# Kernel tuning notes

Measured on AMD Instinct MI355X. Metric: run time of the kernel, lower is better.

Reference implementation:

```python
import jax, jax.numpy as jnp
import numpy as np

WS = 7            # window size
HEADS = 4
DIM = 128         # hidden_dim
HEAD_DIM = 128    # wrapper passes head_dim=hidden_dim (faithful to source)
INNER = HEADS * HEAD_DIM   # 512
MLP = 4 * DIM
PATCH = 4
DISP = WS // 2
NEG = -1e9


def _ln(x, g, b, eps=1e-5):
    m = jnp.mean(x, -1, keepdims=True)
    v = jnp.mean((x - m) ** 2, -1, keepdims=True)
    return (x - m) * jax.lax.rsqrt(v + eps) * g + b


_coords = np.stack(np.meshgrid(np.arange(WS), np.arange(WS), indexing='ij'), -1).reshape(-1, 2)
REL_IDX = jnp.asarray(_coords[None] - _coords[:, None] + WS - 1)  # (ws^2, ws^2, 2)


def _build_masks():
    n = WS * WS
    ul = np.zeros((n, n), np.float32)
    ul[-DISP * WS:, : -DISP * WS] = NEG
    ul[: -DISP * WS, -DISP * WS:] = NEG
    lr = np.zeros((WS, WS, WS, WS), np.float32)
    lr[:, -DISP:, :, : -DISP] = NEG
    lr[:, : -DISP, :, -DISP:] = NEG
    return jnp.asarray(ul), jnp.asarray(lr.reshape(n, n))

UL_MASK, LR_MASK = _build_masks()


def _win_attn(x, w_qkv, pos, w_o, b_o, shifted):
    b, H, W, _ = x.shape
    if shifted:
        x = jnp.roll(x, (-DISP, -DISP), axis=(1, 2))
    nh, nw = H // WS, W // WS
    qkv = x @ w_qkv  # (b, H, W, 3*INNER)

    def to_win(t):  # -> (b, heads, n_windows, ws*ws, head_dim)
        t = t.reshape(b, nh, WS, nw, WS, HEADS, HEAD_DIM)
        return t.transpose(0, 5, 1, 3, 2, 4, 6).reshape(b, HEADS, nh * nw, WS * WS, HEAD_DIM)

    q, k, v = map(to_win, jnp.split(qkv, 3, axis=-1))
    dots = jnp.einsum('bhwid,bhwjd->bhwij', q, k) * (HEAD_DIM ** -0.5)
    dots = dots + pos[REL_IDX[..., 0], REL_IDX[..., 1]]  # shared across heads (berniwal)
    if shifted:
        dots = dots.at[:, :, -nw:].add(UL_MASK)
        dots = dots.at[:, :, nw - 1::nw].add(LR_MASK)
    attn = jax.nn.softmax(dots, axis=-1)
    out = jnp.einsum('bhwij,bhwjd->bhwid', attn, v)
    out = out.reshape(b, HEADS, nh, nw, WS, WS, HEAD_DIM).transpose(0, 2, 4, 3, 5, 1, 6)
    out = out.reshape(b, H, W, INNER) @ w_o + b_o
    if shifted:
        out = jnp.roll(out, (DISP, DISP), axis=(1, 2))
    return out


def _block(x, ga1, be1, w_qkv, pos, w_o, b_o, ga2, be2, w1, b1, w2, b2, shifted):
    x = x + _win_attn(_ln(x, ga1, be1), w_qkv, pos, w_o, b_o, shifted)
    h = jax.nn.gelu(_ln(x, ga2, be2) @ w1 + b1, approximate=False) @ w2 + b2
    return x + h


def _patch_embed(x, w, b):  # Unfold(patch) + Linear, channel-major feature order
    B, C, H, W = x.shape
    nh, nw = H // PATCH, W // PATCH
    x = x.reshape(B, C, nh, PATCH, nw, PATCH).transpose(0, 2, 4, 1, 3, 5)
    return x.reshape(B, nh, nw, C * PATCH * PATCH) @ w + b


def setup_inputs() -> dict:
    key = jax.random.key(0)
    ks = iter(jax.random.split(key, 48))

    def nrm(shape, s=0.02):
        return jax.random.normal(next(ks), shape, dtype=jnp.float32) * s

    inp = {'x': jax.random.normal(next(ks), (32, 3, 224, 224), dtype=jnp.float32)}
    inp['w_pe'] = nrm((3 * PATCH * PATCH, DIM))
    inp['b_pe'] = jnp.zeros((DIM,), jnp.float32)
    for s in ('a', 'b'):
        inp['ga1_' + s] = jnp.ones((DIM,), jnp.float32)
        inp['be1_' + s] = jnp.zeros((DIM,), jnp.float32)
        inp['w_qkv_' + s] = nrm((DIM, 3 * INNER))
        inp['pos_' + s] = nrm((2 * WS - 1, 2 * WS - 1), 1.0)
        inp['w_o_' + s] = nrm((INNER, DIM))
        inp['b_o_' + s] = jnp.zeros((DIM,), jnp.float32)
        inp['ga2_' + s] = jnp.ones((DIM,), jnp.float32)
        inp['be2_' + s] = jnp.zeros((DIM,), jnp.float32)
        inp['w_m1_' + s] = nrm((DIM, MLP))
        inp['b_m1_' + s] = jnp.zeros((MLP,), jnp.float32)
        inp['w_m2_' + s] = nrm((MLP, DIM))
        inp['b_m2_' + s] = jnp.zeros((DIM,), jnp.float32)
    return inp


def reference(x, w_pe, b_pe,
              ga1_a, be1_a, w_qkv_a, pos_a, w_o_a, b_o_a, ga2_a, be2_a, w_m1_a, b_m1_a, w_m2_a, b_m2_a,
              ga1_b, be1_b, w_qkv_b, pos_b, w_o_b, b_o_b, ga2_b, be2_b, w_m1_b, b_m1_b, w_m2_b, b_m2_b):
    h = _patch_embed(x, w_pe, b_pe)  # (B, 56, 56, DIM)
    h = _block(h, ga1_a, be1_a, w_qkv_a, pos_a, w_o_a, b_o_a, ga2_a, be2_a, w_m1_a, b_m1_a, w_m2_a, b_m2_a, False)
    h = _block(h, ga1_b, be1_b, w_qkv_b, pos_b, w_o_b, b_o_b, ga2_b, be2_b, w_m1_b, b_m1_b, w_m2_b, b_m2_b, True)
    return h
```

## Files before the change

### kernel.cpp

```cpp
#include <hip/hip_runtime.h>

typedef __attribute__((ext_vector_type(8))) short bf16x8;
typedef __attribute__((ext_vector_type(4))) short bf16x4;
typedef __attribute__((ext_vector_type(4))) float f32x4;

#define MFMA16(a, b, c) __builtin_amdgcn_mfma_f32_16x16x32_bf16(a, b, c, 0, 0, 0)

static __device__ __forceinline__ short f2bf(float f) {
    union { float f; unsigned u; } x; x.f = f;
    unsigned r = x.u + 0x7FFFu + ((x.u >> 16) & 1u);
    return (short)(r >> 16);
}

static __device__ __forceinline__ void gload16(const void* g, void* l) {
    __builtin_amdgcn_global_load_lds((const __attribute__((address_space(1))) void*)g,
                                     (__attribute__((address_space(3))) void*)l, 16, 0, 0);
}

__global__ void convT_kernel(const float* __restrict__ in, short* __restrict__ out, int K, int N) {
    int idx = blockIdx.x * 256 + threadIdx.x;
    if (idx < K * N) {
        int k = idx % K, n = idx / K;
        out[idx] = f2bf(in[(size_t)k * N + n]);
    }
}

__global__ void tabgen_kernel(const float* __restrict__ pos_a, const float* __restrict__ pos_b,
                              float* __restrict__ tab) {
    int v = blockIdx.x;
    const float* pos = (v == 0) ? pos_a : pos_b;
    for (int e = threadIdx.x; e < 4096; e += 256) {
        int row = e >> 6, key = e & 63;
        float val;
        if (key >= 49) val = -1e9f;
        else if (row >= 49) val = 0.f;
        else {
            int qi = row / 7, qj = row - qi * 7, ki = key / 7, kj = key - ki * 7;
            val = pos[(ki - qi + 6) * 13 + (kj - qj + 6)];
            if (v >= 1) {
                bool wh7 = (v - 1) & 2, ww7 = (v - 1) & 1;
                if (wh7 && ((qi >= 4) != (ki >= 4))) val += -1e9f;
                if (ww7 && ((qj >= 4) != (kj >= 4))) val += -1e9f;
            }
        }
        tab[v * 4096 + e] = val;
    }
}

__global__ __launch_bounds__(256) void patchln_kernel(const float* __restrict__ x,
                                                      const float* __restrict__ w,
                                                      const float* __restrict__ bias,
                                                      const float* __restrict__ g,
                                                      const float* __restrict__ bta,
                                                      float* __restrict__ out,
                                                      short* __restrict__ xn) {
    __shared__ float s_in[2][48];
    __shared__ float red[2][2][2];
    const int tid = threadIdx.x;
    const int half = tid >> 7, c = tid & 127;
    const int winh = (tid >> 6) & 1, lane = tid & 63;
    const int t = blockIdx.x * 2 + half;
    const int b = t / 3136, rem = t - b * 3136;
    const int hp = rem / 56, wp = rem - hp * 56;
    if (c < 48) {
        int cin = c >> 4, py = (c >> 2) & 3, px = c & 3;
        s_in[half][c] = x[((size_t)(b * 3 + cin) * 224 + hp * 4 + py) * 224 + wp * 4 + px];
    }
    __syncthreads();
    float acc = bias[c];
#pragma unroll
    for (int k = 0; k < 48; ++k) acc += s_in[half][k] * w[k * 128 + c];
    out[(size_t)t * 128 + c] = acc;
    float s1 = acc, s2 = acc * acc;
#pragma unroll
    for (int o = 32; o > 0; o >>= 1) { s1 += __shfl_xor(s1, o); s2 += __shfl_xor(s2, o); }
    if (lane == 0) { red[half][winh][0] = s1; red[half][winh][1] = s2; }
    __syncthreads();
    s1 = red[half][0][0] + red[half][1][0];
    s2 = red[half][0][1] + red[half][1][1];
    float mean = s1 * (1.f / 128.f);
    float var = s2 * (1.f / 128.f) - mean * mean;
    float rstd = rsqrtf(var + 1e-5f);
    xn[(size_t)t * 128 + c] = f2bf((acc - mean) * rstd * g[c] + bta[c]);
}

template <int SHIFTED>
__global__ __launch_bounds__(256, 3) void attn_kernel(const short* __restrict__ xn,
                                                      const short* __restrict__ wqkvT,
                                                      const float* __restrict__ tab,
                                                      const short* __restrict__ zpad,
                                                      short* __restrict__ aout) {
    __shared__ short smem[24576];
    short* s_x = smem;
    short* s_q = smem + 8192;
    short* s_k = smem + 16384;
    short* s_vT = smem + 8192;
    short* s_p = smem + 16384;

    const int tid = threadIdx.x;
    const int wid = tid >> 6, lane = tid & 63;
    const int l15 = lane & 15, l4 = lane >> 4, klo = l4 * 8;
    const int bid = blockIdx.x;
    const int win = bid & 63, head = (bid >> 6) & 3, b = bid >> 8;
    const int wh = win >> 3, ww = win & 7;

#pragma unroll
    for (int it = 0; it < 4; ++it) {
        int slot = it * 256 + tid;
        int row = slot >> 4, scol = slot & 15;
        int colb = (scol * 16) ^ ((row & 7) << 4);
        const char* g;
        if (row < 49) {
            int wi = row / 7, wj = row - wi * 7;
            int hh = wh * 7 + wi, wp = ww * 7 + wj;
            if (SHIFTED) { hh += 3; if (hh >= 56) hh -= 56; wp += 3; if (wp >= 56) wp -= 56; }
            int t = (b * 56 + hh) * 56 + wp;
            g = (const char*)(xn + (size_t)t * 128) + colb;
        } else {
            g = (const char*)zpad + colb;
        }
        gload16(g, (char*)smem + (it * 256 + wid * 64) * 16);
    }
    __syncthreads();

    const f32x4 zero4 = {0.f, 0.f, 0.f, 0.f};

    {
        const short* Wq = wqkvT + (size_t)(head * 128) * 128;
        const short* Wk = wqkvT + (size_t)(512 + head * 128) * 128;
        f32x4 aq[2][4], ak[2][4];
#pragma unroll
        for (int mw = 0; mw < 2; ++mw)
#pragma unroll
            for (int j = 0; j < 4; ++j) { aq[mw][j] = zero4; ak[mw][j] = zero4; }
#pragma unroll
        for (int k0 = 0; k0 < 4; ++k0) {
            bf16x8 bx[4], awq[2], awk[2];
#pragma unroll
            for (int j = 0; j < 4; ++j) {
                int row = j * 16 + l15;
                bx[j] = *(const bf16x8*)((const char*)s_x + row * 256 + ((k0 * 64 + l4 * 16) ^ ((row & 7) << 4)));
            }
#pragma unroll
            for (int mw = 0; mw < 2; ++mw) {
                awq[mw] = *(const bf16x8*)(Wq + (size_t)(wid * 32 + mw * 16 + l15) * 128 + k0 * 32 + klo);
                awk[mw] = *(const bf16x8*)(Wk + (size_t)(wid * 32 + mw * 16 + l15) * 128 + k0 * 32 + klo);
            }
            __builtin_amdgcn_s_setprio(1);
#pragma unroll
            for (int mw = 0; mw < 2; ++mw)
#pragma unroll
                for (int j = 0; j < 4; ++j) {
                    aq[mw][j] = MFMA16(awq[mw], bx[j], aq[mw][j]);
                    ak[mw][j] = MFMA16(awk[mw], bx[j], ak[mw][j]);
                }
            __builtin_amdgcn_s_setprio(0);
        }
#pragma unroll
        for (int mw = 0; mw < 2; ++mw)
#pragma unroll
            for (int j = 0; j < 4; ++j) {
                bf16x4 pq, pk;
#pragma unroll
                for (int r = 0; r < 4; ++r) { pq[r] = f2bf(aq[mw][j][r]); pk[r] = f2bf(ak[mw][j][r]); }
                int row = j * 16 + l15;
                int colb = (wid * 64 + mw * 32 + l4 * 8) ^ ((row & 7) << 4);
                *(bf16x4*)((char*)s_q + row * 256 + colb) = pq;
                *(bf16x4*)((char*)s_k + row * 256 + colb) = pk;
            }
    }
    __syncthreads();

    const int qrow = wid * 16 + l15;
    f32x4 dt[4];
#pragma unroll
    for (int m = 0; m < 4; ++m) dt[m] = zero4;
#pragma unroll
    for (int k0 = 0; k0 < 4; ++k0) {
        bf16x8 bq = *(const bf16x8*)((const char*)s_q + qrow * 256 + ((k0 * 64 + l4 * 16) ^ ((qrow & 7) << 4)));
        __builtin_amdgcn_s_setprio(1);
#pragma unroll
        for (int m = 0; m < 4; ++m) {
            int krow = m * 16 + l15;
            bf16x8 akf = *(const bf16x8*)((const char*)s_k + krow * 256 + ((k0 * 64 + l4 * 16) ^ ((krow & 7) << 4)));
            dt[m] = MFMA16(akf, bq, dt[m]);
        }
        __builtin_amdgcn_s_setprio(0);
    }
    __syncthreads();

    const int variant = SHIFTED ? (1 + ((wh == 7) ? 2 : 0) + ((ww == 7) ? 1 : 0)) : 0;
    const float* tv = tab + variant * 4096 + qrow * 64;
    const float SC = 0.08838834764831845f;
    float p[4][4];
    float mx = -3.0e38f;
#pragma unroll
    for (int m = 0; m < 4; ++m) {
        f32x4 tb = *(const f32x4*)(tv + m * 16 + l4 * 4);
#pragma unroll
        for (int r = 0; r < 4; ++r) {
            float d = dt[m][r] * SC + tb[r];
            p[m][r] = d;
            mx = fmaxf(mx, d);
        }
    }
    mx = fmaxf(mx, __shfl_xor(mx, 16));
    mx = fmaxf(mx, __shfl_xor(mx, 32));
    float sum = 0.f;
#pragma unroll
    for (int m = 0; m < 4; ++m)
#pragma unroll
        for (int r = 0; r < 4; ++r) { p[m][r] = __expf(p[m][r] - mx); sum += p[m][r]; }
    sum += __shfl_xor(sum, 16);
    sum += __shfl_xor(sum, 32);
    float inv = 1.f / sum;
#pragma unroll
    for (int m = 0; m < 4; ++m) {
        bf16x4 pv;
#pragma unroll
        for (int r = 0; r < 4; ++r) pv[r] = f2bf(p[m][r] * inv);
        *(bf16x4*)((char*)s_p + qrow * 128 + ((m * 32 + l4 * 8) ^ ((qrow & 7) << 4))) = pv;
    }

    {
        const short* Wv = wqkvT + (size_t)(1024 + head * 128) * 128;
        f32x4 acc[4][2];
#pragma unroll
        for (int m = 0; m < 4; ++m)
#pragma unroll
            for (int n = 0; n < 2; ++n) acc[m][n] = zero4;
#pragma unroll
        for (int k0 = 0; k0 < 4; ++k0) {
            bf16x8 ax[4], bw[2];
#pragma unroll
            for (int m = 0; m < 4; ++m) {
                int row = m * 16 + l15;
                ax[m] = *(const bf16x8*)((const char*)s_x + row * 256 + ((k0 * 64 + l4 * 16) ^ ((row & 7) << 4)));
            }
#pragma unroll
            for (int n = 0; n < 2; ++n)
                bw[n] = *(const bf16x8*)(Wv + (size_t)(wid * 32 + n * 16 + l15) * 128 + k0 * 32 + klo);
            __builtin_amdgcn_s_setprio(1);
#pragma unroll
            for (int m = 0; m < 4; ++m)
#pragma unroll
                for (int n = 0; n < 2; ++n) acc[m][n] = MFMA16(ax[m], bw[n], acc[m][n]);
            __builtin_amdgcn_s_setprio(0);
        }
#pragma unroll
        for (int m = 0; m < 4; ++m)
#pragma unroll
            for (int n = 0; n < 2; ++n) {
                bf16x4 pv;
#pragma unroll
                for (int r = 0; r < 4; ++r) pv[r] = f2bf(acc[m][n][r]);
                int hd = wid * 32 + n * 16 + l15;
                int colb = (m * 32 + l4 * 8) ^ ((hd & 7) << 4);
                *(bf16x4*)((char*)s_vT + hd * 128 + colb) = pv;
            }
    }
    __syncthreads();

    f32x4 o[4][2];
#pragma unroll
    for (int m = 0; m < 4; ++m)
#pragma unroll
        for (int n = 0; n < 2; ++n) o[m][n] = zero4;
#pragma unroll
    for (int k0 = 0; k0 < 2; ++k0) {
        bf16x8 ap[4], bv[2];
#pragma unroll
        for (int m = 0; m < 4; ++m) {
            int row = m * 16 + l15;
            ap[m] = *(const bf16x8*)((const char*)s_p + row * 128 + ((k0 * 64 + l4 * 16) ^ ((row & 7) << 4)));
        }
#pragma unroll
        for (int n = 0; n < 2; ++n) {
            int hd = wid * 32 + n * 16 + l15;
            bv[n] = *(const bf16x8*)((const char*)s_vT + hd * 128 + ((k0 * 64 + l4 * 16) ^ ((hd & 7) << 4)));
        }
        __builtin_amdgcn_s_setprio(1);
#pragma unroll
        for (int m = 0; m < 4; ++m)
#pragma unroll
            for (int n = 0; n < 2; ++n) o[m][n] = MFMA16(ap[m], bv[n], o[m][n]);
        __builtin_amdgcn_s_setprio(0);
    }
#pragma unroll
    for (int m = 0; m < 4; ++m) {
#pragma unroll
        for (int r = 0; r < 4; ++r) {
            int rl = m * 16 + l4 * 4 + r;
            if (rl < 49) {
                int wi = rl / 7, wj = rl - wi * 7;
                int hh = wh * 7 + wi, wp = ww * 7 + wj;
                if (SHIFTED) { hh += 3; if (hh >= 56) hh -= 56; wp += 3; if (wp >= 56) wp -= 56; }
                size_t t = (size_t)(b * 56 + hh) * 56 + wp;
                aout[t * 512 + head * 128 + wid * 32 + l15] = f2bf(o[m][0][r]);
                aout[t * 512 + head * 128 + wid * 32 + 16 + l15] = f2bf(o[m][1][r]);
            }
        }
    }
}

template <int K, int MODE>
__global__ __launch_bounds__(256, 2) void gemm2_kernel(const short* __restrict__ A,
                                                       const short* __restrict__ BT,
                                                       const float* __restrict__ bias,
                                                       const float* __restrict__ resid,
                                                       const float* __restrict__ g,
                                                       const float* __restrict__ bta,
                                                       float* __restrict__ outf,
                                                       short* __restrict__ outb,
                                                       int Ntot) {
    __shared__ char smem[32768];
    short* s_a = (short*)smem;
    short* s_b = (short*)(smem + 16384);
    float* red = (float*)smem;

    const int tid = threadIdx.x, wid = tid >> 6, lane = tid & 63;
    const int wr = wid >> 1, wc = wid & 1;
    const int l15 = lane & 15, l4 = lane >> 4;
    const int m0 = blockIdx.x * 128;
    const int nb0 = blockIdx.y * 128;

    const f32x4 zero4 = {0.f, 0.f, 0.f, 0.f};
    f32x4 acc[4][4];
#pragma unroll
    for (int m = 0; m < 4; ++m)
#pragma unroll
        for (int n = 0; n < 4; ++n) acc[m][n] = zero4;

    for (int kc = 0; kc < K / 64; ++kc) {
#pragma unroll
        for (int it = 0; it < 4; ++it) {
            int slot = it * 256 + tid;
            int row = slot >> 3, scol = slot & 7;
            int colb = (scol * 16) ^ ((row & 7) << 4);
            gload16((const char*)(A + (size_t)(m0 + row) * K + kc * 64) + colb,
                    (char*)smem + (it * 256 + wid * 64) * 16);
        }
#pragma unroll
        for (int it = 0; it < 4; ++it) {
            int slot = it * 256 + tid;
            int row = slot >> 3, scol = slot & 7;
            int colb = (scol * 16) ^ ((row & 7) << 4);
            gload16((const char*)(BT + (size_t)(nb0 + row) * K + kc * 64) + colb,
                    (char*)smem + 16384 + (it * 256 + wid * 64) * 16);
        }
        __syncthreads();
#pragma unroll
        for (int ks = 0; ks < 2; ++ks) {
            bf16x8 a[4], bfr[4];
#pragma unroll
            for (int m = 0; m < 4; ++m) {
                int row = wr * 64 + m * 16 + l15;
                a[m] = *(const bf16x8*)((const char*)s_a + row * 128 + ((ks * 64 + l4 * 16) ^ ((row & 7) << 4)));
            }
#pragma unroll
            for (int n = 0; n < 4; ++n) {
                int row = wc * 64 + n * 16 + l15;
                bfr[n] = *(const bf16x8*)((const char*)s_b + row * 128 + ((ks * 64 + l4 * 16) ^ ((row & 7) << 4)));
            }
            __builtin_amdgcn_s_setprio(1);
#pragma unroll
            for (int m = 0; m < 4; ++m)
#pragma unroll
                for (int n = 0; n < 4; ++n) acc[m][n] = MFMA16(a[m], bfr[n], acc[m][n]);
            __builtin_amdgcn_s_setprio(0);
        }
        __syncthreads();
    }

    float bv[4];
#pragma unroll
    for (int n = 0; n < 4; ++n) bv[n] = bias[nb0 + wc * 64 + n * 16 + l15];

    if (MODE == 0) {
#pragma unroll
        for (int m = 0; m < 4; ++m)
#pragma unroll
            for (int r = 0; r < 4; ++r) {
                int row = m0 + wr * 64 + m * 16 + l4 * 4 + r;
#pragma unroll
                for (int n = 0; n < 4; ++n) {
                    int col = nb0 + wc * 64 + n * 16 + l15;
                    float v = acc[m][n][r] + bv[n];
                    v = 0.5f * v * (1.f + erff(v * 0.70710678118f));
                    outb[(size_t)row * Ntot + col] = f2bf(v);
                }
            }
        return;
    }

    float s1[4][4], s2[4][4];
#pragma unroll
    for (int m = 0; m < 4; ++m)
#pragma unroll
        for (int r = 0; r < 4; ++r) {
            int row = m0 + wr * 64 + m * 16 + l4 * 4 + r;
            float a1 = 0.f, a2 = 0.f;
#pragma unroll
            for (int n = 0; n < 4; ++n) {
                int col = wc * 64 + n * 16 + l15;
                float v = acc[m][n][r] + bv[n] + resid[(size_t)row * 128 + col];
                acc[m][n][r] = v;
                a1 += v; a2 += v * v;
            }
            s1[m][r] = a1; s2[m][r] = a2;
        }

    if (MODE == 1) {
#pragma unroll
        for (int m = 0; m < 4; ++m)
#pragma unroll
            for (int r = 0; r < 4; ++r) {
#pragma unroll
                for (int o = 1; o < 16; o <<= 1) {
                    s1[m][r] += __shfl_xor(s1[m][r], o);
                    s2[m][r] += __shfl_xor(s2[m][r], o);
                }
            }
        __syncthreads();
#pragma unroll
        for (int m = 0; m < 4; ++m)
#pragma unroll
            for (int r = 0; r < 4; ++r) {
                if (l15 == m * 4 + r) {
                    int lrow = wr * 64 + m * 16 + l4 * 4 + r;
                    red[lrow * 4 + wc * 2] = s1[m][r];
                    red[lrow * 4 + wc * 2 + 1] = s2[m][r];
                }
            }
        __syncthreads();
    }

#pragma unroll
    for (int m = 0; m < 4; ++m)
#pragma unroll
        for (int r = 0; r < 4; ++r) {
            int lrow = wr * 64 + m * 16 + l4 * 4 + r;
            int row = m0 + lrow;
            float mean = 0.f, rstd = 0.f;
            if (MODE == 1) {
                float t1 = red[lrow * 4] + red[lrow * 4 + 2];
                float t2 = red[lrow * 4 + 1] + red[lrow * 4 + 3];
                mean = t1 * (1.f / 128.f);
                float var = t2 * (1.f / 128.f) - mean * mean;
                rstd = rsqrtf(var + 1e-5f);
            }
#pragma unroll
            for (int n = 0; n < 4; ++n) {
                int col = wc * 64 + n * 16 + l15;
                float v = acc[m][n][r];
                outf[(size_t)row * 128 + col] = v;
                if (MODE == 1)
                    outb[(size_t)row * 128 + col] = f2bf((v - mean) * rstd * g[col] + bta[col]);
            }
        }
}

extern "C" void kernel_launch(void* const* d_in, const int* in_sizes, int n_in,
                              void* d_out, int out_size, void* d_ws, size_t ws_size,
                              hipStream_t stream) {
    const float* x = (const float*)d_in[0];
    const float* w_pe = (const float*)d_in[1];
    const float* b_pe = (const float*)d_in[2];
    const float* P[24];
    for (int i = 0; i < 24; ++i) P[i] = (const float*)d_in[3 + i];

    float* out = (float*)d_out;
    const size_t TOK = 100352;

    short* xn = (short*)d_ws;
    short* abuf = xn + TOK * 128;
    short* wqkv = abuf + TOK * 512;
    short* wo = wqkv + 196608;
    short* wm1 = wo + 65536;
    short* wm2 = wm1 + 65536;
    float* tab = (float*)(wm2 + 65536);
    short* zpad = (short*)(tab + 5 * 4096);

    hipMemsetAsync(zpad, 0, 256, stream);
    tabgen_kernel<<<5, 256, 0, stream>>>(P[3], P[15], tab);

    patchln_kernel<<<50176, 256, 0, stream>>>(x, w_pe, b_pe, P[0], P[1], out, xn);

    for (int s = 0; s < 2; ++s) {
        convT_kernel<<<768, 256, 0, stream>>>(P[s * 12 + 2], wqkv, 128, 1536);
        convT_kernel<<<256, 256, 0, stream>>>(P[s * 12 + 4], wo, 512, 128);
        convT_kernel<<<256, 256, 0, stream>>>(P[s * 12 + 8], wm1, 128, 512);
        convT_kernel<<<256, 256, 0, stream>>>(P[s * 12 + 10], wm2, 512, 128);

        if (s == 0)
            attn_kernel<0><<<8192, 256, 0, stream>>>(xn, wqkv, tab, zpad, abuf);
        else
            attn_kernel<1><<<8192, 256, 0, stream>>>(xn, wqkv, tab, zpad, abuf);

        gemm2_kernel<512, 1><<<dim3(784, 1), 256, 0, stream>>>(
            abuf, wo, P[s * 12 + 5], out, P[s * 12 + 6], P[s * 12 + 7], out, xn, 128);

        gemm2_kernel<128, 0><<<dim3(784, 4), 256, 0, stream>>>(
            xn, wm1, P[s * 12 + 9], nullptr, nullptr, nullptr, nullptr, abuf, 512);

        if (s == 0)
            gemm2_kernel<512, 1><<<dim3(784, 1), 256, 0, stream>>>(
                abuf, wm2, P[11], out, P[12], P[13], out, xn, 128);
        else
            gemm2_kernel<512, 2><<<dim3(784, 1), 256, 0, stream>>>(
                abuf, wm2, P[23], out, nullptr, nullptr, out, nullptr, 128);
    }
}
```

Measured before the change: 624.2 us.

## Restructure window attention: compute V early, drop a barrier, vectorize output stores

The V projection now runs right after the Q/K projection, in the same phase, and its transposed result is written over the s_x buffer. The softmax probabilities go into the s_q region, which removes one __syncthreads. The P·V MFMA swaps its operands so each lane holds four contiguous head-dim values, so output stores become 8-byte vector writes instead of scattered 2-byte ones, using precomputed token rows. Float-to-bf16 conversion uses the hardware v_cvt_pk_bf16_f32 instruction, and divisions by 7 become multiply-shift. V's accumulators stay live across the QK phase, which raises register pressure and may hurt the 3-waves occupancy target.

```diff
diff --git a/kernel.cpp b/kernel.cpp
--- a/kernel.cpp
+++ b/kernel.cpp
@@ -3,6 +3,7 @@
 typedef __attribute__((ext_vector_type(8))) short bf16x8;
 typedef __attribute__((ext_vector_type(4))) short bf16x4;
 typedef __attribute__((ext_vector_type(4))) float f32x4;
+typedef __attribute__((ext_vector_type(2))) unsigned u32x2;
 
 #define MFMA16(a, b, c) __builtin_amdgcn_mfma_f32_16x16x32_bf16(a, b, c, 0, 0, 0)
 
@@ -10,6 +11,12 @@
     union { float f; unsigned u; } x; x.f = f;
     unsigned r = x.u + 0x7FFFu + ((x.u >> 16) & 1u);
     return (short)(r >> 16);
+}
+
+static __device__ __forceinline__ unsigned cvtpk(float lo, float hi) {
+    unsigned r;
+    asm("v_cvt_pk_bf16_f32 %0, %1, %2" : "=v"(r) : "v"(lo), "v"(hi));
+    return r;
 }
 
 static __device__ __forceinline__ void gload16(const void* g, void* l) {
@@ -94,8 +101,6 @@
     short* s_x = smem;
     short* s_q = smem + 8192;
     short* s_k = smem + 16384;
-    short* s_vT = smem + 8192;
-    short* s_p = smem + 16384;
 
     const int tid = threadIdx.x;
     const int wid = tid >> 6, lane = tid & 63;
@@ -104,6 +109,16 @@
     const int win = bid & 63, head = (bid >> 6) & 3, b = bid >> 8;
     const int wh = win >> 3, ww = win & 7;
 
+    int trow[4];
+#pragma unroll
+    for (int j = 0; j < 4; ++j) {
+        int r = j * 16 + l15; r = (r > 48) ? 48 : r;
+        int wi = (r * 37) >> 8, wj = r - wi * 7;
+        int hh = wh * 7 + wi, wp = ww * 7 + wj;
+        if (SHIFTED) { hh += 3; if (hh >= 56) hh -= 56; wp += 3; if (wp >= 56) wp -= 56; }
+        trow[j] = (b * 56 + hh) * 56 + wp;
+    }
+
 #pragma unroll
     for (int it = 0; it < 4; ++it) {
         int slot = it * 256 + tid;
@@ -111,7 +126,7 @@
         int colb = (scol * 16) ^ ((row & 7) << 4);
         const char* g;
         if (row < 49) {
-            int wi = row / 7, wj = row - wi * 7;
+            int wi = (row * 37) >> 8, wj = row - wi * 7;
             int hh = wh * 7 + wi, wp = ww * 7 + wj;
             if (SHIFTED) { hh += 3; if (hh >= 56) hh -= 56; wp += 3; if (wp >= 56) wp -= 56; }
             int t = (b * 56 + hh) * 56 + wp;
@@ -160,16 +175,51 @@
         for (int mw = 0; mw < 2; ++mw)
 #pragma unroll
             for (int j = 0; j < 4; ++j) {
-                bf16x4 pq, pk;
-#pragma unroll
-                for (int r = 0; r < 4; ++r) { pq[r] = f2bf(aq[mw][j][r]); pk[r] = f2bf(ak[mw][j][r]); }
+                u32x2 pq = { cvtpk(aq[mw][j][0], aq[mw][j][1]), cvtpk(aq[mw][j][2], aq[mw][j][3]) };
+                u32x2 pk = { cvtpk(ak[mw][j][0], ak[mw][j][1]), cvtpk(ak[mw][j][2], ak[mw][j][3]) };
                 int row = j * 16 + l15;
                 int colb = (wid * 64 + mw * 32 + l4 * 8) ^ ((row & 7) << 4);
-                *(bf16x4*)((char*)s_q + row * 256 + colb) = pq;
-                *(bf16x4*)((char*)s_k + row * 256 + colb) = pk;
-            }
+                *(u32x2*)((char*)s_q + row * 256 + colb) = pq;
+                *(u32x2*)((char*)s_k + row * 256 + colb) = pk;
+            }
+    }
+
+    f32x4 av[4][2];
+#pragma unroll
+    for (int m = 0; m < 4; ++m)
+#pragma unroll
+        for (int n = 0; n < 2; ++n) av[m][n] = zero4;
+    {
+        const short* Wv = wqkvT + (size_t)(1024 + head * 128) * 128;
+#pragma unroll
+        for (int k0 = 0; k0 < 4; ++k0) {
+            bf16x8 ax[4], bw[2];
+#pragma unroll
+            for (int m = 0; m < 4; ++m) {
+                int row = m * 16 + l15;
+                ax[m] = *(const bf16x8*)((const char*)s_x + row * 256 + ((k0 * 64 + l4 * 16) ^ ((row & 7) << 4)));
+            }
+#pragma unroll
+            for (int n = 0; n < 2; ++n)
+                bw[n] = *(const bf16x8*)(Wv + (size_t)(wid * 32 + n * 16 + l15) * 128 + k0 * 32 + klo);
+            __builtin_amdgcn_s_setprio(1);
+#pragma unroll
+            for (int m = 0; m < 4; ++m)
+#pragma unroll
+                for (int n = 0; n < 2; ++n) av[m][n] = MFMA16(ax[m], bw[n], av[m][n]);
+            __builtin_amdgcn_s_setprio(0);
+        }
     }
     __syncthreads();
+
+#pragma unroll
+    for (int m = 0; m < 4; ++m)
+#pragma unroll
+        for (int n = 0; n < 2; ++n) {
+            u32x2 pv = { cvtpk(av[m][n][0], av[m][n][1]), cvtpk(av[m][n][2], av[m][n][3]) };
+            int hd = wid * 32 + n * 16 + l15;
+            *(u32x2*)((char*)s_x + hd * 128 + ((m * 32 + l4 * 8) ^ ((hd & 7) << 4))) = pv;
+        }
 
     const int qrow = wid * 16 + l15;
     f32x4 dt[4];
@@ -187,7 +237,6 @@
         }
         __builtin_amdgcn_s_setprio(0);
     }
-    __syncthreads();
 
     const int variant = SHIFTED ? (1 + ((wh == 7) ? 2 : 0) + ((ww == 7) ? 1 : 0)) : 0;
     const float* tv = tab + variant * 4096 + qrow * 64;
@@ -216,88 +265,44 @@
     float inv = 1.f / sum;
 #pragma unroll
     for (int m = 0; m < 4; ++m) {
-        bf16x4 pv;
-#pragma unroll
-        for (int r = 0; r < 4; ++r) pv[r] = f2bf(p[m][r] * inv);
-        *(bf16x4*)((char*)s_p + qrow * 128 + ((m * 32 + l4 * 8) ^ ((qrow & 7) << 4))) = pv;
-    }
-
-    {
-        const short* Wv = wqkvT + (size_t)(1024 + head * 128) * 128;
-        f32x4 acc[4][2];
-#pragma unroll
-        for (int m = 0; m < 4; ++m)
-#pragma unroll
-            for (int n = 0; n < 2; ++n) acc[m][n] = zero4;
-#pragma unroll
-        for (int k0 = 0; k0 < 4; ++k0) {
-            bf16x8 ax[4], bw[2];
-#pragma unroll
-            for (int m = 0; m < 4; ++m) {
-                int row = m * 16 + l15;
-                ax[m] = *(const bf16x8*)((const char*)s_x + row * 256 + ((k0 * 64 + l4 * 16) ^ ((row & 7) << 4)));
-            }
-#pragma unroll
-            for (int n = 0; n < 2; ++n)
-                bw[n] = *(const bf16x8*)(Wv + (size_t)(wid * 32 + n * 16 + l15) * 128 + k0 * 32 + klo);
-            __builtin_amdgcn_s_setprio(1);
-#pragma unroll
-            for (int m = 0; m < 4; ++m)
-#pragma unroll
-                for (int n = 0; n < 2; ++n) acc[m][n] = MFMA16(ax[m], bw[n], acc[m][n]);
-            __builtin_amdgcn_s_setprio(0);
-        }
-#pragma unroll
-        for (int m = 0; m < 4; ++m)
-#pragma unroll
-            for (int n = 0; n < 2; ++n) {
-                bf16x4 pv;
-#pragma unroll
-                for (int r = 0; r < 4; ++r) pv[r] = f2bf(acc[m][n][r]);
-                int hd = wid * 32 + n * 16 + l15;
-                int colb = (m * 32 + l4 * 8) ^ ((hd & 7) << 4);
-                *(bf16x4*)((char*)s_vT + hd * 128 + colb) = pv;
-            }
+        u32x2 pv = { cvtpk(p[m][0] * inv, p[m][1] * inv), cvtpk(p[m][2] * inv, p[m][3] * inv) };
+        *(u32x2*)((char*)s_q + qrow * 256 + ((m * 32 + l4 * 8) ^ ((qrow & 7) << 4))) = pv;
     }
     __syncthreads();
 
-    f32x4 o[4][2];
-#pragma unroll
-    for (int m = 0; m < 4; ++m)
-#pragma unroll
-        for (int n = 0; n < 2; ++n) o[m][n] = zero4;
+    f32x4 o[2][4];
+#pragma unroll
+    for (int fn = 0; fn < 2; ++fn)
+#pragma unroll
+        for (int tm = 0; tm < 4; ++tm) o[fn][tm] = zero4;
 #pragma unroll
     for (int k0 = 0; k0 < 2; ++k0) {
-        bf16x8 ap[4], bv[2];
-#pragma unroll
-        for (int m = 0; m < 4; ++m) {
-            int row = m * 16 + l15;
-            ap[m] = *(const bf16x8*)((const char*)s_p + row * 128 + ((k0 * 64 + l4 * 16) ^ ((row & 7) << 4)));
-        }
-#pragma unroll
-        for (int n = 0; n < 2; ++n) {
-            int hd = wid * 32 + n * 16 + l15;
-            bv[n] = *(const bf16x8*)((const char*)s_vT + hd * 128 + ((k0 * 64 + l4 * 16) ^ ((hd & 7) << 4)));
+        bf16x8 ap[4], bv2[2];
+#pragma unroll
+        for (int tm = 0; tm < 4; ++tm) {
+            int row = tm * 16 + l15;
+            ap[tm] = *(const bf16x8*)((const char*)s_q + row * 256 + ((k0 * 64 + l4 * 16) ^ ((row & 7) << 4)));
+        }
+#pragma unroll
+        for (int fn = 0; fn < 2; ++fn) {
+            int hd = wid * 32 + fn * 16 + l15;
+            bv2[fn] = *(const bf16x8*)((const char*)s_x + hd * 128 + ((k0 * 64 + l4 * 16) ^ ((hd & 7) << 4)));
         }
         __builtin_amdgcn_s_setprio(1);
 #pragma unroll
-        for (int m = 0; m < 4; ++m)
-#pragma unroll
-            for (int n = 0; n < 2; ++n) o[m][n] = MFMA16(ap[m], bv[n], o[m][n]);
+        for (int fn = 0; fn < 2; ++fn)
+#pragma unroll
+            for (int tm = 0; tm < 4; ++tm) o[fn][tm] = MFMA16(bv2[fn], ap[tm], o[fn][tm]);
         __builtin_amdgcn_s_setprio(0);
     }
 #pragma unroll
-    for (int m = 0; m < 4; ++m) {
-#pragma unroll
-        for (int r = 0; r < 4; ++r) {
-            int rl = m * 16 + l4 * 4 + r;
-            if (rl < 49) {
-                int wi = rl / 7, wj = rl - wi * 7;
-                int hh = wh * 7 + wi, wp = ww * 7 + wj;
-                if (SHIFTED) { hh += 3; if (hh >= 56) hh -= 56; wp += 3; if (wp >= 56) wp -= 56; }
-                size_t t = (size_t)(b * 56 + hh) * 56 + wp;
-                aout[t * 512 + head * 128 + wid * 32 + l15] = f2bf(o[m][0][r]);
-                aout[t * 512 + head * 128 + wid * 32 + 16 + l15] = f2bf(o[m][1][r]);
+    for (int tm = 0; tm < 4; ++tm) {
+        if (tm * 16 + l15 < 49) {
+            short* dst = aout + (size_t)trow[tm] * 512 + head * 128 + wid * 32 + l4 * 4;
+#pragma unroll
+            for (int fn = 0; fn < 2; ++fn) {
+                u32x2 pv = { cvtpk(o[fn][tm][0], o[fn][tm][1]), cvtpk(o[fn][tm][2], o[fn][tm][3]) };
+                *(u32x2*)(dst + fn * 16) = pv;
             }
         }
     }
```

New measurement: 640.0 us. 1.03x slower.
